# Performance work log

Measured on AMD Instinct MI355X. Metric: run time of the kernel, lower is better.

## Reference

```python
import jax, jax.numpy as jnp
import numpy as np

S, B, D = 2048, 2, 1024
H, DH = 16, 64  # heads, dim_head; H*DH == D (required by out.view)
SCALE = DH ** -0.5


def setup_inputs() -> dict:
    key = jax.random.key(0)
    ks = jax.random.split(key, 9)
    s = 0.02
    return {
        "x": jax.random.normal(ks[0], (S, B, D), jnp.float32),
        "Wq": jax.random.normal(ks[1], (H * DH, D), jnp.float32) * s,
        "bq": jax.random.normal(ks[2], (H * DH,), jnp.float32) * s,
        "Wk": jax.random.normal(ks[3], (H * DH, D), jnp.float32) * s,
        "bk": jax.random.normal(ks[4], (H * DH,), jnp.float32) * s,
        "Wv": jax.random.normal(ks[5], (H * DH, D), jnp.float32) * s,
        "bv": jax.random.normal(ks[6], (H * DH,), jnp.float32) * s,
        "Wo": jax.random.normal(ks[7], (D, H * DH), jnp.float32) * s,
        "bo": jax.random.normal(ks[8], (D,), jnp.float32) * s,
    }


def reference(x, Wq, bq, Wk, bk, Wv, bv, Wo, bo):
    # x: [S, B, D] (seq-first, matching the torch module)
    q = (x @ Wq.T + bq).reshape(S, B, H, DH)
    k = (x @ Wk.T + bk).reshape(S, B, H, DH)
    v = (x @ Wv.T + bv).reshape(S, B, H, DH)
    # scores: [B, H, S, S]
    dots = jnp.einsum("sbhd,tbhd->bhst", q, k) * SCALE
    attn = jax.nn.softmax(dots, axis=-1)  # dropout p=0.0 -> identity
    out = jnp.einsum("bhst,tbhd->sbhd", attn, v).reshape(S, B, H * DH)
    return out @ Wo.T + bo
```

## Files before the change

### kernel.cpp

```cpp
#include <hip/hip_runtime.h>
#include <hip/hip_bf16.h>

typedef unsigned short u16;
typedef unsigned int u32;
typedef __bf16 bf16x8 __attribute__((ext_vector_type(8)));
typedef float f32x4 __attribute__((ext_vector_type(4)));
typedef float f32x16 __attribute__((ext_vector_type(16)));

static constexpr int kS = 2048;
static constexpr int kB = 2;
static constexpr int kD = 1024;
static constexpr int kDH = 64;
static constexpr int kM = kS * kB;
static constexpr float kScale = 0.125f;
static constexpr float kLog2e = 1.44269504088896340736f;

__device__ __forceinline__ u16 f2bf(float f) {
  return __builtin_bit_cast(u16, static_cast<__bf16>(f));
}

__device__ __forceinline__ u32 pack2(float lo, float hi) {
  union { u16 h[2]; u32 u; } x;
  x.h[0] = f2bf(lo); x.h[1] = f2bf(hi);
  return x.u;
}

__device__ __forceinline__ void permswap(u32& a, u32& b) {
  asm volatile("v_permlane32_swap_b32 %0, %1" : "+v"(a), "+v"(b));
}

__device__ __forceinline__ float exp2_hw(float x) {
  float r;
  asm("v_exp_f32 %0, %1" : "=v"(r) : "v"(x));
  return r;
}

__device__ __forceinline__ void load_lds16(const void* g, void* l) {
  __builtin_amdgcn_global_load_lds(
      (const __attribute__((address_space(1))) void*)g,
      (__attribute__((address_space(3))) void*)l, 16, 0, 0);
}

__global__ void cast_f32_bf16(const float* __restrict__ in, u16* __restrict__ out, int n) {
  int i = (blockIdx.x * blockDim.x + threadIdx.x) * 4;
  const int stride = gridDim.x * blockDim.x * 4;
  for (; i < n; i += stride) {
    const float4 v = *reinterpret_cast<const float4*>(in + i);
    ushort4 o;
    o.x = f2bf(v.x); o.y = f2bf(v.y); o.z = f2bf(v.z); o.w = f2bf(v.w);
    *reinterpret_cast<ushort4*>(out + i) = o;
  }
}

__global__ void cast_w4(const float* __restrict__ Wq, const float* __restrict__ Wk,
                        const float* __restrict__ Wv, const float* __restrict__ Wo,
                        u16* __restrict__ dq, u16* __restrict__ dk,
                        u16* __restrict__ dv, u16* __restrict__ dw) {
  const float* src; u16* dst;
  switch (blockIdx.y) {
    case 0: src = Wq; dst = dq; break;
    case 1: src = Wk; dst = dk; break;
    case 2: src = Wv; dst = dv; break;
    default: src = Wo; dst = dw; break;
  }
  const int i = (blockIdx.x * blockDim.x + threadIdx.x) * 4;
  const float4 v = *reinterpret_cast<const float4*>(src + i);
  ushort4 o;
  o.x = f2bf(v.x); o.y = f2bf(v.y); o.z = f2bf(v.z); o.w = f2bf(v.w);
  *reinterpret_cast<ushort4*>(dst + i) = o;
}

template <int MODE>
__device__ __forceinline__ void gemm_body(
    const u16* __restrict__ A, const u16* __restrict__ W,
    const float* __restrict__ bias, void* __restrict__ Out,
    int M, int N, int K, float oscale) {
  __shared__ u16 As[128 * 64];
  __shared__ u16 Bs[128 * 64];
  const int tid = threadIdx.x;
  const int lane = tid & 63;
  const int wid = tid >> 6;
  const int wr = (wid >> 2) * 64;
  const int wc = (wid & 3) * 32;
  const int l15 = lane & 15;
  const int lg = lane >> 4;
  const int tm = blockIdx.x * 128;
  const int tn = blockIdx.y * 128;

  auto stage = [&](int k0) {
#pragma unroll
    for (int p = 0; p < 2; ++p) {
      const int c = p * 512 + tid;
      const int row = c >> 3;
      const int scc = (c & 7) ^ (row & 7);
      load_lds16(A + (size_t)(tm + row) * K + k0 + scc * 8, &As[c * 8]);
      load_lds16(W + (size_t)(tn + row) * K + k0 + scc * 8, &Bs[c * 8]);
    }
  };

  f32x4 acc[4][2] = {};

#pragma unroll 1
  for (int ks = 0; ks < K / 64; ++ks) {
    stage(ks * 64);
    __syncthreads();
#pragma unroll
    for (int kh = 0; kh < 2; ++kh) {
      bf16x8 af[4], bw[2];
#pragma unroll
      for (int i = 0; i < 4; ++i) {
        const int row = wr + i * 16 + l15;
        af[i] = *reinterpret_cast<const bf16x8*>(
            &As[row * 64 + (((kh * 4 + lg) ^ (row & 7)) * 8)]);
      }
#pragma unroll
      for (int j = 0; j < 2; ++j) {
        const int row = wc + j * 16 + l15;
        bw[j] = *reinterpret_cast<const bf16x8*>(
            &Bs[row * 64 + (((kh * 4 + lg) ^ (row & 7)) * 8)]);
      }
#pragma unroll
      for (int i = 0; i < 4; ++i)
#pragma unroll
        for (int j = 0; j < 2; ++j)
          acc[i][j] = __builtin_amdgcn_mfma_f32_16x16x32_bf16(af[i], bw[j], acc[i][j], 0, 0, 0);
    }
    __syncthreads();
  }

#pragma unroll
  for (int i = 0; i < 4; ++i)
#pragma unroll
    for (int j = 0; j < 2; ++j)
#pragma unroll
      for (int r = 0; r < 4; ++r) {
        const int row = tm + wr + i * 16 + lg * 4 + r;
        const int col = tn + wc + j * 16 + l15;
        const float v = (acc[i][j][r] + bias[col]) * oscale;
        if constexpr (MODE == 0) {
          reinterpret_cast<u16*>(Out)[(size_t)row * N + col] = f2bf(v);
        } else if constexpr (MODE == 1) {
          reinterpret_cast<float*>(Out)[(size_t)row * N + col] = v;
        } else {
          const int s_ = row >> 1, b_ = row & 1;
          const int h_ = col >> 6, dh_ = col & 63;
          reinterpret_cast<u16*>(Out)[((size_t)(b_ * 16 + h_) * 64 + dh_) * kS + s_] = f2bf(v);
        }
      }
}

__global__ __launch_bounds__(512, 6) void qkv_gemm(
    const u16* __restrict__ xb,
    const u16* __restrict__ Wqb, const u16* __restrict__ Wkb, const u16* __restrict__ Wvb,
    const float* __restrict__ bq, const float* __restrict__ bk, const float* __restrict__ bv,
    u16* __restrict__ Q, u16* __restrict__ K, u16* __restrict__ Vt) {
  const int z = blockIdx.z;
  if (z == 2) {
    gemm_body<2>(xb, Wvb, bv, Vt, kM, kD, kD, 1.0f);
  } else if (z == 0) {
    gemm_body<0>(xb, Wqb, bq, Q, kM, kD, kD, kScale * kLog2e);
  } else {
    gemm_body<0>(xb, Wkb, bk, K, kM, kD, kD, 1.0f);
  }
}

__global__ __launch_bounds__(512, 6) void out_gemm(
    const u16* __restrict__ Ob, const u16* __restrict__ Wob,
    const float* __restrict__ bo, float* __restrict__ out) {
  gemm_body<1>(Ob, Wob, bo, out, kM, kD, kD, 1.0f);
}

__global__ __launch_bounds__(512, 4) void attn_fwd(
    const u16* __restrict__ Qg, const u16* __restrict__ Kg,
    const u16* __restrict__ Vtg, u16* __restrict__ Og) {
  __shared__ u16 Ksm[2][2][64 * 64];
  __shared__ u16 Vsm[2][2][64 * 64];

  const int tid = threadIdx.x;
  const int lane = tid & 63;
  const int w = tid >> 6;
  const int half = w >> 2;
  const int wsub = w & 3;
  const int ltid = tid & 255;
  const int l31 = lane & 31;
  const int hi = lane >> 5;

  const int bid = blockIdx.x;
  const int xcd = bid & 7;
  const int idx = bid >> 3;
  const int bh = xcd * 4 + (idx & 3);
  const int qb = idx >> 2;
  const int b = bh & 1;
  const int h = bh >> 1;
  const int hoff = h * kDH;
  const int vslot = b * 16 + h;
  const int qrow = qb * 128 + wsub * 32 + l31;

  bf16x8 qf[4];
#pragma unroll
  for (int ks = 0; ks < 4; ++ks)
    qf[ks] = *reinterpret_cast<const bf16x8*>(
        &Qg[(size_t)(qrow * kB + b) * kD + hoff + ks * 16 + hi * 8]);

  f32x16 acc[2] = {};
  float lac[4] = {0.f, 0.f, 0.f, 0.f};

  auto stage = [&](int t0, int buf) {
#pragma unroll
    for (int p = 0; p < 2; ++p) {
      const int c = p * 256 + ltid;
      const int row = c >> 3;
      const int cc = c & 7;
      const int scc = cc ^ (row & 7);
      load_lds16(&Kg[(size_t)((t0 + row) * kB + b) * kD + hoff + scc * 8],
                 &Ksm[half][buf][c * 8]);
      load_lds16(&Vtg[(size_t)(vslot * 64 + row) * kS + t0 + scc * 8],
                 &Vsm[half][buf][c * 8]);
    }
  };

  const int tbase = half * 16;
  stage(tbase * 64, 0);

#pragma unroll 1
  for (int ti = 0; ti < 16; ++ti) {
    asm volatile("s_waitcnt vmcnt(0)" ::: "memory");
    __builtin_amdgcn_sched_barrier(0);
    __builtin_amdgcn_s_barrier();
    __builtin_amdgcn_sched_barrier(0);
    if (ti + 1 < 16) stage((tbase + ti + 1) * 64, (ti + 1) & 1);

    const int cur = ti & 1;

    f32x16 sc[2] = {};
    __builtin_amdgcn_s_setprio(1);
#pragma unroll
    for (int nb = 0; nb < 2; ++nb) {
      const int krow = nb * 32 + l31;
#pragma unroll
      for (int ks = 0; ks < 4; ++ks) {
        const bf16x8 kf = *reinterpret_cast<const bf16x8*>(
            &Ksm[half][cur][krow * 64 + (((ks * 2 + hi) ^ (krow & 7)) * 8)]);
        sc[nb] = __builtin_amdgcn_mfma_f32_32x32x16_bf16(kf, qf[ks], sc[nb], 0, 0, 0);
      }
    }
    __builtin_amdgcn_s_setprio(0);

    bf16x8 pb[4];
#pragma unroll
    for (int nb = 0; nb < 2; ++nb) {
      float p[16];
#pragma unroll
      for (int r = 0; r < 16; ++r) {
        p[r] = exp2_hw(sc[nb][r]);
        lac[r & 3] += p[r];
      }
      u32 pk[4][2];
#pragma unroll
      for (int q = 0; q < 4; ++q)
#pragma unroll
        for (int w2 = 0; w2 < 2; ++w2)
          pk[q][w2] = pack2(p[4 * q + 2 * w2], p[4 * q + 2 * w2 + 1]);
#pragma unroll
      for (int k1 = 0; k1 < 2; ++k1) {
        u32 a0 = pk[2 * k1][0], b0 = pk[2 * k1 + 1][0];
        u32 a1 = pk[2 * k1][1], b1 = pk[2 * k1 + 1][1];
        permswap(a0, b0);
        permswap(a1, b1);
        union { u32 wv[4]; bf16x8 v; } U;
        U.wv[0] = a0; U.wv[1] = a1; U.wv[2] = b0; U.wv[3] = b1;
        pb[2 * nb + k1] = U.v;
      }
    }

    __builtin_amdgcn_s_setprio(1);
#pragma unroll
    for (int ks = 0; ks < 4; ++ks)
#pragma unroll
      for (int n2 = 0; n2 < 2; ++n2) {
        const int vrow = n2 * 32 + l31;
        const bf16x8 va = *reinterpret_cast<const bf16x8*>(
            &Vsm[half][cur][vrow * 64 + (((ks * 2 + hi) ^ (vrow & 7)) * 8)]);
        acc[n2] = __builtin_amdgcn_mfma_f32_32x32x16_bf16(va, pb[ks], acc[n2], 0, 0, 0);
      }
    __builtin_amdgcn_s_setprio(0);
  }

  __syncthreads();
  float* Ocmb = reinterpret_cast<float*>(&Ksm[0][0][0]);
  float* Lcmb = reinterpret_cast<float*>(&Vsm[0][0][0]);
  const float l_own = (lac[0] + lac[1]) + (lac[2] + lac[3]);
  const float l_half = l_own + __shfl_xor(l_own, 32);
  const int q = wsub * 32 + l31;

  if (half == 1) {
    if (hi == 0) Lcmb[q] = l_half;
#pragma unroll
    for (int n2 = 0; n2 < 2; ++n2)
#pragma unroll
      for (int q4 = 0; q4 < 4; ++q4)
#pragma unroll
        for (int rp = 0; rp < 2; ++rp) {
          const int dh0 = n2 * 32 + q4 * 8 + hi * 4 + rp * 2;
          const int a = q * 64 + (dh0 ^ ((l31 & 7) << 3));
          *reinterpret_cast<float2*>(&Ocmb[a]) =
              make_float2(acc[n2][q4 * 4 + rp * 2], acc[n2][q4 * 4 + rp * 2 + 1]);
        }
  }
  __syncthreads();
  if (half == 0) {
    const float inv = 1.0f / (l_half + Lcmb[q]);
#pragma unroll
    for (int n2 = 0; n2 < 2; ++n2)
#pragma unroll
      for (int q4 = 0; q4 < 4; ++q4)
#pragma unroll
        for (int rp = 0; rp < 2; ++rp) {
          const int dh0 = n2 * 32 + q4 * 8 + hi * 4 + rp * 2;
          const int a = q * 64 + (dh0 ^ ((l31 & 7) << 3));
          const float2 o = *reinterpret_cast<const float2*>(&Ocmb[a]);
          acc[n2][q4 * 4 + rp * 2]     += o.x;
          acc[n2][q4 * 4 + rp * 2 + 1] += o.y;
        }
#pragma unroll
    for (int n2 = 0; n2 < 2; ++n2)
#pragma unroll
      for (int g = 0; g < 4; ++g) {
        const int dh0 = n2 * 32 + g * 8 + hi * 4;
        ushort4 o;
        o.x = f2bf(acc[n2][g * 4 + 0] * inv);
        o.y = f2bf(acc[n2][g * 4 + 1] * inv);
        o.z = f2bf(acc[n2][g * 4 + 2] * inv);
        o.w = f2bf(acc[n2][g * 4 + 3] * inv);
        *reinterpret_cast<ushort4*>(&Og[(size_t)(qrow * kB + b) * kD + hoff + dh0]) = o;
      }
  }
}

extern "C" void kernel_launch(void* const* d_in, const int* in_sizes, int n_in,
                              void* d_out, int out_size, void* d_ws, size_t ws_size,
                              hipStream_t stream) {
  const float* x  = (const float*)d_in[0];
  const float* Wq = (const float*)d_in[1];
  const float* bq = (const float*)d_in[2];
  const float* Wk = (const float*)d_in[3];
  const float* bk = (const float*)d_in[4];
  const float* Wv = (const float*)d_in[5];
  const float* bv = (const float*)d_in[6];
  const float* Wo = (const float*)d_in[7];
  const float* bo = (const float*)d_in[8];
  float* out = (float*)d_out;

  char* ws = (char*)d_ws;
  u16* xb  = (u16*)(ws + 0);
  u16* Wqb = (u16*)(ws + 8388608);
  u16* Wkb = (u16*)(ws + 10485760);
  u16* Wvb = (u16*)(ws + 12582912);
  u16* Wob = (u16*)(ws + 14680064);
  u16* Qb  = (u16*)(ws + 16777216);
  u16* Kb  = (u16*)(ws + 25165824);
  u16* Vtb = (u16*)(ws + 33554432);
  u16* Ob  = (u16*)(ws + 41943040);

  cast_f32_bf16<<<4096, 256, 0, stream>>>(x, xb, kM * kD);
  cast_w4<<<dim3(1024, 4), 256, 0, stream>>>(Wq, Wk, Wv, Wo, Wqb, Wkb, Wvb, Wob);

  qkv_gemm<<<dim3(kM / 128, kD / 128, 3), 512, 0, stream>>>(
      xb, Wqb, Wkb, Wvb, bq, bk, bv, Qb, Kb, Vtb);

  attn_fwd<<<512, 512, 0, stream>>>(Qb, Kb, Vtb, Ob);

  out_gemm<<<dim3(kM / 128, kD / 128), 512, 0, stream>>>(Ob, Wob, bo, out);
}
```

Measured before the change: 118.3 us.

## Software-pipeline attention loop by overlapping QK of next tile with PV of previous

Restructures the attention inner loop so each iteration computes the QK scores for tile i while running the PV MFMAs for tile i-1, interleaving softmax halves with PV halves. The V shared-memory buffer becomes triple-buffered with rotating indices, the loop is unrolled by two to alternate the P register sets, and a prologue and epilogue handle the first and last tiles. The aim is to hide exp and pack latency behind matrix work and keep the MFMA units busier. In exchange, LDS use grows from 64KB to 80KB per block and register pressure rises from holding two P fragment sets at once.

```diff
diff --git a/kernel.cpp b/kernel.cpp
--- a/kernel.cpp
+++ b/kernel.cpp
@@ -173,8 +173,8 @@
 __global__ __launch_bounds__(512, 4) void attn_fwd(
     const u16* __restrict__ Qg, const u16* __restrict__ Kg,
     const u16* __restrict__ Vtg, u16* __restrict__ Og) {
-  __shared__ u16 Ksm[2][2][64 * 64];
-  __shared__ u16 Vsm[2][2][64 * 64];
+  __shared__ u16 Ksm[2 * 2 * 4096];
+  __shared__ u16 Vsm[2 * 3 * 4096];
 
   const int tid = threadIdx.x;
   const int lane = tid & 63;
@@ -196,6 +196,9 @@
   const int vslot = b * 16 + h;
   const int qrow = qb * 128 + wsub * 32 + l31;
 
+  u16* Kh = &Ksm[half * 2 * 4096];
+  u16* Vh = &Vsm[half * 3 * 4096];
+
   bf16x8 qf[4];
 #pragma unroll
   for (int ks = 0; ks < 4; ++ks)
@@ -205,90 +208,122 @@
   f32x16 acc[2] = {};
   float lac[4] = {0.f, 0.f, 0.f, 0.f};
 
-  auto stage = [&](int t0, int buf) {
+  auto stage = [&](int t0, int kbuf, int vbuf) {
 #pragma unroll
     for (int p = 0; p < 2; ++p) {
       const int c = p * 256 + ltid;
       const int row = c >> 3;
-      const int cc = c & 7;
-      const int scc = cc ^ (row & 7);
+      const int scc = (c & 7) ^ (row & 7);
       load_lds16(&Kg[(size_t)((t0 + row) * kB + b) * kD + hoff + scc * 8],
-                 &Ksm[half][buf][c * 8]);
+                 &Kh[kbuf * 4096 + c * 8]);
       load_lds16(&Vtg[(size_t)(vslot * 64 + row) * kS + t0 + scc * 8],
-                 &Vsm[half][buf][c * 8]);
+                 &Vh[vbuf * 4096 + c * 8]);
     }
   };
 
+  auto qk = [&](int kbuf, f32x16 (&sc)[2]) {
+    __builtin_amdgcn_s_setprio(1);
+#pragma unroll
+    for (int nb = 0; nb < 2; ++nb) {
+      const int krow = nb * 32 + l31;
+#pragma unroll
+      for (int ks = 0; ks < 4; ++ks) {
+        const bf16x8 kf = *reinterpret_cast<const bf16x8*>(
+            &Kh[kbuf * 4096 + krow * 64 + (((ks * 2 + hi) ^ (krow & 7)) * 8)]);
+        sc[nb] = __builtin_amdgcn_mfma_f32_32x32x16_bf16(kf, qf[ks], sc[nb], 0, 0, 0);
+      }
+    }
+    __builtin_amdgcn_s_setprio(0);
+  };
+
+  auto smhalf = [&](f32x16 (&sc)[2], bf16x8 (&pb)[4], int nb) {
+    float p[16];
+#pragma unroll
+    for (int r = 0; r < 16; ++r) {
+      p[r] = exp2_hw(sc[nb][r]);
+      lac[r & 3] += p[r];
+    }
+    u32 pk[4][2];
+#pragma unroll
+    for (int q = 0; q < 4; ++q)
+#pragma unroll
+      for (int w2 = 0; w2 < 2; ++w2)
+        pk[q][w2] = pack2(p[4 * q + 2 * w2], p[4 * q + 2 * w2 + 1]);
+#pragma unroll
+    for (int k1 = 0; k1 < 2; ++k1) {
+      u32 a0 = pk[2 * k1][0], b0 = pk[2 * k1 + 1][0];
+      u32 a1 = pk[2 * k1][1], b1 = pk[2 * k1 + 1][1];
+      permswap(a0, b0);
+      permswap(a1, b1);
+      union { u32 wv[4]; bf16x8 v; } U;
+      U.wv[0] = a0; U.wv[1] = a1; U.wv[2] = b0; U.wv[3] = b1;
+      pb[2 * nb + k1] = U.v;
+    }
+  };
+
+  auto pvhalf = [&](int vbuf, bf16x8 (&pb)[4], int ks0) {
+    __builtin_amdgcn_s_setprio(1);
+#pragma unroll
+    for (int ks = ks0; ks < ks0 + 2; ++ks)
+#pragma unroll
+      for (int n2 = 0; n2 < 2; ++n2) {
+        const int vrow = n2 * 32 + l31;
+        const bf16x8 va = *reinterpret_cast<const bf16x8*>(
+            &Vh[vbuf * 4096 + vrow * 64 + (((ks * 2 + hi) ^ (vrow & 7)) * 8)]);
+        acc[n2] = __builtin_amdgcn_mfma_f32_32x32x16_bf16(va, pb[ks], acc[n2], 0, 0, 0);
+      }
+    __builtin_amdgcn_s_setprio(0);
+  };
+
+  bf16x8 pbE[4], pbO[4];
   const int tbase = half * 16;
-  stage(tbase * 64, 0);
-
-#pragma unroll 1
-  for (int ti = 0; ti < 16; ++ti) {
+  int vb_prev = 0, vb_cur = 1, vb_next = 2;
+
+  stage(tbase * 64, 0, 0);
+
+  {
     asm volatile("s_waitcnt vmcnt(0)" ::: "memory");
     __builtin_amdgcn_sched_barrier(0);
     __builtin_amdgcn_s_barrier();
     __builtin_amdgcn_sched_barrier(0);
-    if (ti + 1 < 16) stage((tbase + ti + 1) * 64, (ti + 1) & 1);
-
-    const int cur = ti & 1;
-
+    stage((tbase + 1) * 64, 1, 1);
     f32x16 sc[2] = {};
-    __builtin_amdgcn_s_setprio(1);
-#pragma unroll
-    for (int nb = 0; nb < 2; ++nb) {
-      const int krow = nb * 32 + l31;
-#pragma unroll
-      for (int ks = 0; ks < 4; ++ks) {
-        const bf16x8 kf = *reinterpret_cast<const bf16x8*>(
-            &Ksm[half][cur][krow * 64 + (((ks * 2 + hi) ^ (krow & 7)) * 8)]);
-        sc[nb] = __builtin_amdgcn_mfma_f32_32x32x16_bf16(kf, qf[ks], sc[nb], 0, 0, 0);
-      }
-    }
-    __builtin_amdgcn_s_setprio(0);
-
-    bf16x8 pb[4];
-#pragma unroll
-    for (int nb = 0; nb < 2; ++nb) {
-      float p[16];
-#pragma unroll
-      for (int r = 0; r < 16; ++r) {
-        p[r] = exp2_hw(sc[nb][r]);
-        lac[r & 3] += p[r];
-      }
-      u32 pk[4][2];
-#pragma unroll
-      for (int q = 0; q < 4; ++q)
-#pragma unroll
-        for (int w2 = 0; w2 < 2; ++w2)
-          pk[q][w2] = pack2(p[4 * q + 2 * w2], p[4 * q + 2 * w2 + 1]);
-#pragma unroll
-      for (int k1 = 0; k1 < 2; ++k1) {
-        u32 a0 = pk[2 * k1][0], b0 = pk[2 * k1 + 1][0];
-        u32 a1 = pk[2 * k1][1], b1 = pk[2 * k1 + 1][1];
-        permswap(a0, b0);
-        permswap(a1, b1);
-        union { u32 wv[4]; bf16x8 v; } U;
-        U.wv[0] = a0; U.wv[1] = a1; U.wv[2] = b0; U.wv[3] = b1;
-        pb[2 * nb + k1] = U.v;
-      }
-    }
-
-    __builtin_amdgcn_s_setprio(1);
-#pragma unroll
-    for (int ks = 0; ks < 4; ++ks)
-#pragma unroll
-      for (int n2 = 0; n2 < 2; ++n2) {
-        const int vrow = n2 * 32 + l31;
-        const bf16x8 va = *reinterpret_cast<const bf16x8*>(
-            &Vsm[half][cur][vrow * 64 + (((ks * 2 + hi) ^ (vrow & 7)) * 8)]);
-        acc[n2] = __builtin_amdgcn_mfma_f32_32x32x16_bf16(va, pb[ks], acc[n2], 0, 0, 0);
-      }
-    __builtin_amdgcn_s_setprio(0);
-  }
+    qk(0, sc);
+    smhalf(sc, pbE, 0);
+    smhalf(sc, pbE, 1);
+  }
+
+#define ATTN_BODY(TI, KBUF, PB_CUR, PB_PREV)                              \
+  {                                                                       \
+    asm volatile("s_waitcnt vmcnt(0)" ::: "memory");                      \
+    __builtin_amdgcn_sched_barrier(0);                                    \
+    __builtin_amdgcn_s_barrier();                                         \
+    __builtin_amdgcn_sched_barrier(0);                                    \
+    if ((TI) < 15) stage((tbase + (TI) + 1) * 64, (KBUF) ^ 1, vb_next);   \
+    f32x16 sc[2] = {};                                                    \
+    qk((KBUF), sc);                                                       \
+    pvhalf(vb_prev, PB_PREV, 0);                                          \
+    smhalf(sc, PB_CUR, 0);                                                \
+    pvhalf(vb_prev, PB_PREV, 2);                                          \
+    smhalf(sc, PB_CUR, 1);                                                \
+    const int t_ = vb_prev; vb_prev = vb_cur; vb_cur = vb_next; vb_next = t_; \
+  }
+
+#pragma unroll 1
+  for (int k2 = 0; k2 < 7; ++k2) {
+    const int ti = 2 * k2 + 1;
+    ATTN_BODY(ti, 1, pbO, pbE)
+    ATTN_BODY(ti + 1, 0, pbE, pbO)
+  }
+  ATTN_BODY(15, 1, pbO, pbE)
+#undef ATTN_BODY
+
+  pvhalf(vb_prev, pbO, 0);
+  pvhalf(vb_prev, pbO, 2);
 
   __syncthreads();
-  float* Ocmb = reinterpret_cast<float*>(&Ksm[0][0][0]);
-  float* Lcmb = reinterpret_cast<float*>(&Vsm[0][0][0]);
+  float* Ocmb = reinterpret_cast<float*>(&Ksm[0]);
+  float* Lcmb = reinterpret_cast<float*>(&Vsm[0]);
   const float l_own = (lac[0] + lac[1]) + (lac[2] + lac[3]);
   const float l_half = l_own + __shfl_xor(l_own, 32);
   const int q = wsub * 32 + l31;
```

New measurement: 153.0 us. 1.29x slower.

## Load K and V tiles directly from global memory instead of staging through LDS

Applied to the files above, without the earlier changes.

Removes the double-buffered LDS staging of K and V tiles and the per-iteration barrier. Each wave now loads its MFMA operands straight from global memory, relying on L1/L2 caching since four waves in a half share the same K/V tiles. LDS is kept only for the final cross-half combine. This removes barrier synchronisation, but it adds redundant global traffic, exposes load latency because nothing is prefetched, and raises register pressure.

```diff
diff --git a/kernel.cpp b/kernel.cpp
--- a/kernel.cpp
+++ b/kernel.cpp
@@ -173,15 +173,14 @@
 __global__ __launch_bounds__(512, 4) void attn_fwd(
     const u16* __restrict__ Qg, const u16* __restrict__ Kg,
     const u16* __restrict__ Vtg, u16* __restrict__ Og) {
-  __shared__ u16 Ksm[2][2][64 * 64];
-  __shared__ u16 Vsm[2][2][64 * 64];
+  __shared__ float Ocmb[128 * 64];
+  __shared__ float Lcmb[128];
 
   const int tid = threadIdx.x;
   const int lane = tid & 63;
   const int w = tid >> 6;
   const int half = w >> 2;
   const int wsub = w & 3;
-  const int ltid = tid & 255;
   const int l31 = lane & 31;
   const int hi = lane >> 5;
 
@@ -205,45 +204,29 @@
   f32x16 acc[2] = {};
   float lac[4] = {0.f, 0.f, 0.f, 0.f};
 
-  auto stage = [&](int t0, int buf) {
-#pragma unroll
-    for (int p = 0; p < 2; ++p) {
-      const int c = p * 256 + ltid;
-      const int row = c >> 3;
-      const int cc = c & 7;
-      const int scc = cc ^ (row & 7);
-      load_lds16(&Kg[(size_t)((t0 + row) * kB + b) * kD + hoff + scc * 8],
-                 &Ksm[half][buf][c * 8]);
-      load_lds16(&Vtg[(size_t)(vslot * 64 + row) * kS + t0 + scc * 8],
-                 &Vsm[half][buf][c * 8]);
-    }
-  };
-
   const int tbase = half * 16;
-  stage(tbase * 64, 0);
+  const u16* Kbase = Kg + (size_t)b * kD + hoff;
+  const u16* Vbase = Vtg + (size_t)vslot * 64 * kS;
 
 #pragma unroll 1
   for (int ti = 0; ti < 16; ++ti) {
-    asm volatile("s_waitcnt vmcnt(0)" ::: "memory");
-    __builtin_amdgcn_sched_barrier(0);
-    __builtin_amdgcn_s_barrier();
-    __builtin_amdgcn_sched_barrier(0);
-    if (ti + 1 < 16) stage((tbase + ti + 1) * 64, (ti + 1) & 1);
-
-    const int cur = ti & 1;
+    const int t0 = (tbase + ti) * 64;
+
+    bf16x8 kf[2][4];
+#pragma unroll
+    for (int nb = 0; nb < 2; ++nb)
+#pragma unroll
+      for (int ks = 0; ks < 4; ++ks)
+        kf[nb][ks] = *reinterpret_cast<const bf16x8*>(
+            &Kbase[(size_t)(t0 + nb * 32 + l31) * (kB * kD) + ks * 16 + hi * 8]);
 
     f32x16 sc[2] = {};
     __builtin_amdgcn_s_setprio(1);
 #pragma unroll
-    for (int nb = 0; nb < 2; ++nb) {
-      const int krow = nb * 32 + l31;
-#pragma unroll
-      for (int ks = 0; ks < 4; ++ks) {
-        const bf16x8 kf = *reinterpret_cast<const bf16x8*>(
-            &Ksm[half][cur][krow * 64 + (((ks * 2 + hi) ^ (krow & 7)) * 8)]);
-        sc[nb] = __builtin_amdgcn_mfma_f32_32x32x16_bf16(kf, qf[ks], sc[nb], 0, 0, 0);
-      }
-    }
+    for (int nb = 0; nb < 2; ++nb)
+#pragma unroll
+      for (int ks = 0; ks < 4; ++ks)
+        sc[nb] = __builtin_amdgcn_mfma_f32_32x32x16_bf16(kf[nb][ks], qf[ks], sc[nb], 0, 0, 0);
     __builtin_amdgcn_s_setprio(0);
 
     bf16x8 pb[4];
@@ -273,22 +256,24 @@
       }
     }
 
+    bf16x8 va[2][4];
+#pragma unroll
+    for (int n2 = 0; n2 < 2; ++n2)
+#pragma unroll
+      for (int ks = 0; ks < 4; ++ks)
+        va[n2][ks] = *reinterpret_cast<const bf16x8*>(
+            &Vbase[(size_t)(n2 * 32 + l31) * kS + t0 + ks * 16 + hi * 8]);
+
     __builtin_amdgcn_s_setprio(1);
 #pragma unroll
     for (int ks = 0; ks < 4; ++ks)
 #pragma unroll
-      for (int n2 = 0; n2 < 2; ++n2) {
-        const int vrow = n2 * 32 + l31;
-        const bf16x8 va = *reinterpret_cast<const bf16x8*>(
-            &Vsm[half][cur][vrow * 64 + (((ks * 2 + hi) ^ (vrow & 7)) * 8)]);
-        acc[n2] = __builtin_amdgcn_mfma_f32_32x32x16_bf16(va, pb[ks], acc[n2], 0, 0, 0);
-      }
+      for (int n2 = 0; n2 < 2; ++n2)
+        acc[n2] = __builtin_amdgcn_mfma_f32_32x32x16_bf16(va[n2][ks], pb[ks], acc[n2], 0, 0, 0);
     __builtin_amdgcn_s_setprio(0);
   }
 
   __syncthreads();
-  float* Ocmb = reinterpret_cast<float*>(&Ksm[0][0][0]);
-  float* Lcmb = reinterpret_cast<float*>(&Vsm[0][0][0]);
   const float l_own = (lac[0] + lac[1]) + (lac[2] + lac[3]);
   const float l_half = l_own + __shfl_xor(l_own, 32);
   const int q = wsub * 32 + l31;
```

Result: slower. 189.5 us (+60.3%).
